# Kernel optimization log

Measured on AMD Instinct MI355X. Metric: run time of the kernel, lower is better.

The kernel has to match this reference:

```python
import jax, jax.numpy as jnp
import numpy as np

N_NODES = 100000
N_RELS = 1000
N_EDGES = 400000
DIM = 256  # even: split into real/imag halves


def setup_inputs() -> dict:
    key = jax.random.key(0)
    k1, k2, k3, k4, k5 = jax.random.split(key, 5)
    node_emb = jax.random.normal(k1, (N_NODES, DIM), dtype=jnp.float32)
    rel_emb = jax.random.normal(k2, (N_RELS, DIM), dtype=jnp.float32)
    src = jax.random.randint(k3, (N_EDGES,), 0, N_NODES, dtype=jnp.int64 if jax.config.jax_enable_x64 else jnp.int32).astype(jnp.int32)
    dst = jax.random.randint(k4, (N_EDGES,), 0, N_NODES).astype(jnp.int32)
    rel_id = jax.random.randint(k5, (N_EDGES,), 0, N_RELS).astype(jnp.int32)
    return {"node_emb": node_emb, "rel_emb": rel_emb, "src": src, "dst": dst, "rel_id": rel_id}


def reference(node_emb, rel_emb, src, dst, rel_id):
    h = node_emb[src]      # [E, D] gathered head embeddings
    t = node_emb[dst]      # [E, D] gathered tail embeddings
    r = rel_emb[rel_id]    # [E, D] gathered relation embeddings
    half = h.shape[-1] // 2
    rh, ih = h[:, :half], h[:, half:]
    rt, it = t[:, :half], t[:, half:]
    rr, ir = r[:, :half], r[:, half:]
    # ComplEx: Re(<h, r, conj(t)>)
    score = rh * rt * rr + ih * it * rr + rh * it * ir - ih * rt * ir
    return jnp.sum(score, axis=-1)  # [E]
```

## Files before the change

kernel.cpp:

```cpp
#include <hip/hip_runtime.h>
#include <hip/hip_fp16.h>
#include <string.h>

#define DIM 256

typedef __attribute__((ext_vector_type(2))) _Float16 half2v;

#if defined(__has_builtin)
#if __has_builtin(__builtin_amdgcn_fdot2)
#define HAVE_FDOT2 1
#endif
#endif

__global__ __launch_bounds__(256) void compress_f16i_kernel(
    const float* __restrict__ node, const float* __restrict__ rel,
    int4* __restrict__ out, int n_node, int n_total)
{
    int i = blockIdx.x * blockDim.x + threadIdx.x;
    int row = i >> 5;
    int q   = i & 31;
    if (row >= n_total) return;

    const float* base = (row < n_node)
        ? (node + (size_t)row * DIM)
        : (rel + (size_t)(row - n_node) * DIM);

    float4 a = *((const float4*)base + q);
    float4 b = *((const float4*)(base + 128) + q);

    __half2 p0 = __float22half2_rn(make_float2(a.x, b.x));
    __half2 p1 = __float22half2_rn(make_float2(a.y, b.y));
    __half2 p2 = __float22half2_rn(make_float2(a.z, b.z));
    __half2 p3 = __float22half2_rn(make_float2(a.w, b.w));

    int4 o;
    memcpy(&o.x, &p0, 4);
    memcpy(&o.y, &p1, 4);
    memcpy(&o.z, &p2, 4);
    memcpy(&o.w, &p3, 4);
    out[(size_t)row * 32 + q] = o;
}

__device__ __forceinline__ float pair_term(int h32, int t32, int r32, float acc)
{
    unsigned tu = (unsigned)t32;
    unsigned tsw = (tu >> 16) | ((tu << 16) ^ 0x80000000u);

    half2v h2, t2, r2, ts2;
    memcpy(&h2, &h32, 4);
    memcpy(&t2, &t32, 4);
    memcpy(&r2, &r32, 4);
    memcpy(&ts2, &tsw, 4);

#ifdef HAVE_FDOT2
    float u = __builtin_amdgcn_fdot2(r2, t2, 0.0f, false);
    float v = __builtin_amdgcn_fdot2(r2, ts2, 0.0f, false);
#else
    float rr = (float)r2.x, ir = (float)r2.y;
    float rt = (float)t2.x, it = (float)t2.y;
    float u = rr * rt + ir * it;
    float v = rr * it - ir * rt;
    (void)ts2;
#endif
    float rh = (float)h2.x;
    float ih = (float)h2.y;
    acc = fmaf(rh, u, acc);
    acc = fmaf(ih, v, acc);
    return acc;
}

__global__ __launch_bounds__(256) void complex_score_f16i4_kernel(
    const __half* __restrict__ node,
    const __half* __restrict__ rel,
    const int* __restrict__ src,
    const int* __restrict__ dst,
    const int* __restrict__ rid,
    float* __restrict__ out,
    int n_edges, int quarter)
{
    const int tid  = blockIdx.x * blockDim.x + threadIdx.x;
    const int g    = tid >> 5;
    const int lane = tid & 31;
    if (g >= quarter) return;

    int e[4];
    bool have[4];
    #pragma unroll
    for (int k = 0; k < 4; ++k) {
        e[k] = g + k * quarter;
        have[k] = (e[k] < n_edges);
    }

    int s[4], d[4], r[4];
    #pragma unroll
    for (int k = 0; k < 4; ++k) {
        int ek = have[k] ? e[k] : 0;
        s[k] = src[ek];
        d[k] = dst[ek];
        r[k] = rid[ek];
    }

    const int4* np = (const int4*)node;
    const int4* rp = (const int4*)rel;

    int4 hv[4], tv[4], vv[4];
    #pragma unroll
    for (int k = 0; k < 4; ++k) {
        hv[k] = np[(size_t)s[k] * 32 + lane];
        tv[k] = np[(size_t)d[k] * 32 + lane];
        vv[k] = rp[(size_t)r[k] * 32 + lane];
    }

    float acc[4];
    #pragma unroll
    for (int k = 0; k < 4; ++k) {
        float a = 0.0f;
        a = pair_term(hv[k].x, tv[k].x, vv[k].x, a);
        a = pair_term(hv[k].y, tv[k].y, vv[k].y, a);
        a = pair_term(hv[k].z, tv[k].z, vv[k].z, a);
        a = pair_term(hv[k].w, tv[k].w, vv[k].w, a);
        acc[k] = a;
    }

    #pragma unroll
    for (int off = 16; off > 0; off >>= 1) {
        #pragma unroll
        for (int k = 0; k < 4; ++k)
            acc[k] += __shfl_xor(acc[k], off);
    }

    if (lane == 0) {
        #pragma unroll
        for (int k = 0; k < 4; ++k)
            if (have[k]) out[e[k]] = acc[k];
    }
}

__global__ __launch_bounds__(256) void complex_score_f32_kernel(
    const float* __restrict__ node_emb,
    const float* __restrict__ rel_emb,
    const int* __restrict__ src,
    const int* __restrict__ dst,
    const int* __restrict__ rel_id,
    float* __restrict__ out,
    int n_edges)
{
    const int tid  = blockIdx.x * blockDim.x + threadIdx.x;
    const int edge = tid >> 5;
    const int lane = tid & 31;
    if (edge >= n_edges) return;

    const int s = src[edge];
    const int d = dst[edge];
    const int r = rel_id[edge];

    const float4* hp = (const float4*)(node_emb + (size_t)s * DIM);
    const float4* tp = (const float4*)(node_emb + (size_t)d * DIM);
    const float4* rp = (const float4*)(rel_emb  + (size_t)r * DIM);

    float4 rh = hp[lane];
    float4 ih = hp[lane + 32];
    float4 rt = tp[lane];
    float4 it = tp[lane + 32];
    float4 rr = rp[lane];
    float4 ir = rp[lane + 32];

    float a0 = rr.x * (rh.x * rt.x + ih.x * it.x) + ir.x * (rh.x * it.x - ih.x * rt.x);
    float a1 = rr.y * (rh.y * rt.y + ih.y * it.y) + ir.y * (rh.y * it.y - ih.y * rt.y);
    float a2 = rr.z * (rh.z * rt.z + ih.z * it.z) + ir.z * (rh.z * it.z - ih.z * rt.z);
    float a3 = rr.w * (rh.w * rt.w + ih.w * it.w) + ir.w * (rh.w * it.w - ih.w * rt.w);
    float acc = (a0 + a1) + (a2 + a3);

    #pragma unroll
    for (int off = 16; off > 0; off >>= 1)
        acc += __shfl_xor(acc, off, 32);

    if (lane == 0)
        out[edge] = acc;
}

extern "C" void kernel_launch(void* const* d_in, const int* in_sizes, int n_in,
                              void* d_out, int out_size, void* d_ws, size_t ws_size,
                              hipStream_t stream) {
    const float* node_emb = (const float*)d_in[0];
    const float* rel_emb  = (const float*)d_in[1];
    const int*   src      = (const int*)d_in[2];
    const int*   dst      = (const int*)d_in[3];
    const int*   rel_id   = (const int*)d_in[4];
    float* out = (float*)d_out;

    const int n_edges = in_sizes[2];
    const int n_nodes = in_sizes[0] / DIM;
    const int n_rels  = in_sizes[1] / DIM;

    const size_t f16_bytes = ((size_t)n_nodes + (size_t)n_rels) * DIM * 2;
    const int tpb = 256;

    if (ws_size >= f16_bytes) {
        __half* node_f16 = (__half*)d_ws;
        __half* rel_f16  = node_f16 + (size_t)n_nodes * DIM;

        const int n_total_rows = n_nodes + n_rels;
        const long long comp_threads = (long long)n_total_rows * 32;
        compress_f16i_kernel<<<(int)((comp_threads + tpb - 1) / tpb), tpb, 0, stream>>>(
            node_emb, rel_emb, (int4*)d_ws, n_nodes, n_total_rows);

        const int quarter = (n_edges + 3) / 4;
        const long long score_threads = (long long)quarter * 32;
        complex_score_f16i4_kernel<<<(int)((score_threads + tpb - 1) / tpb), tpb, 0, stream>>>(
            node_f16, rel_f16, src, dst, rel_id, out, n_edges, quarter);
    } else {
        const long long total_threads = (long long)n_edges * 32;
        complex_score_f32_kernel<<<(int)((total_threads + tpb - 1) / tpb), tpb, 0, stream>>>(
            node_emb, rel_emb, src, dst, rel_id, out, n_edges);
    }
}
```

Before: 219.0 us.

## Bucket edges by source node range before scoring to improve gather locality

Adds a coarse counting sort of edges by the high bits of the source index (histogram, scan, scatter into packed int4 records holding src, dst, rel and original edge id). The scoring kernel then reads the packed records, so edges processed close together touch nearby head rows, aiming for better L2/MALL hit rates on the gathers. In exchange it launches four extra small kernels and an extra pass over the index arrays. Only the head gather gains locality; tail and relation gathers stay random.

```diff
diff --git a/kernel.cpp b/kernel.cpp
--- a/kernel.cpp
+++ b/kernel.cpp
@@ -3,6 +3,7 @@
 #include <string.h>
 
 #define DIM 256
+#define CHUNK 2048
 
 typedef __attribute__((ext_vector_type(2))) _Float16 half2v;
 
@@ -39,6 +40,85 @@
     memcpy(&o.z, &p2, 4);
     memcpy(&o.w, &p3, 4);
     out[(size_t)row * 32 + q] = o;
+}
+
+__global__ void zero_cnt_kernel(unsigned* __restrict__ cnt, int nb)
+{
+    int i = threadIdx.x;
+    if (i < nb) cnt[i] = 0u;
+}
+
+__global__ __launch_bounds__(256) void hist_kernel(
+    const int* __restrict__ src, unsigned* __restrict__ cnt,
+    int n_edges, int shift, int nb)
+{
+    __shared__ unsigned lh[64];
+    int tid = threadIdx.x;
+    if (tid < 64) lh[tid] = 0u;
+    __syncthreads();
+
+    int base = blockIdx.x * CHUNK;
+    #pragma unroll
+    for (int i = 0; i < CHUNK / 256; ++i) {
+        int e = base + i * 256 + tid;
+        if (e < n_edges) {
+            int b = src[e] >> shift;
+            atomicAdd(&lh[b], 1u);
+        }
+    }
+    __syncthreads();
+    if (tid < nb && lh[tid]) atomicAdd(&cnt[tid], lh[tid]);
+}
+
+__global__ void scan_kernel(const unsigned* __restrict__ cnt,
+                            unsigned* __restrict__ cursors, int nb)
+{
+    int lane = threadIdx.x;
+    unsigned v = (lane < nb) ? cnt[lane] : 0u;
+    unsigned x = v;
+    #pragma unroll
+    for (int off = 1; off < 64; off <<= 1) {
+        unsigned y = __shfl_up(x, off);
+        if (lane >= off) x += y;
+    }
+    if (lane < nb) cursors[lane] = x - v;
+}
+
+__global__ __launch_bounds__(256) void scatter_kernel(
+    const int* __restrict__ src, const int* __restrict__ dst,
+    const int* __restrict__ rid, unsigned* __restrict__ cursors,
+    int4* __restrict__ packed, int n_edges, int shift, int nb)
+{
+    __shared__ unsigned lh[64];
+    __shared__ unsigned lbase[64];
+    int tid = threadIdx.x;
+    if (tid < 64) lh[tid] = 0u;
+    __syncthreads();
+
+    int base = blockIdx.x * CHUNK;
+    #pragma unroll
+    for (int i = 0; i < CHUNK / 256; ++i) {
+        int e = base + i * 256 + tid;
+        if (e < n_edges) atomicAdd(&lh[src[e] >> shift], 1u);
+    }
+    __syncthreads();
+    if (tid < 64) {
+        unsigned c = lh[tid];
+        lbase[tid] = (tid < nb && c) ? atomicAdd(&cursors[tid], c) : 0u;
+        lh[tid] = 0u;
+    }
+    __syncthreads();
+    #pragma unroll
+    for (int i = 0; i < CHUNK / 256; ++i) {
+        int e = base + i * 256 + tid;
+        if (e < n_edges) {
+            int s = src[e];
+            int b = s >> shift;
+            unsigned rank = atomicAdd(&lh[b], 1u);
+            unsigned pos = lbase[b] + rank;
+            packed[pos] = make_int4(s, dst[e], rid[e], e);
+        }
+    }
 }
 
 __device__ __forceinline__ float pair_term(int h32, int t32, int r32, float acc)
@@ -69,6 +149,68 @@
     return acc;
 }
 
+__global__ __launch_bounds__(256) void complex_score_f16p_kernel(
+    const __half* __restrict__ node,
+    const __half* __restrict__ rel,
+    const int4* __restrict__ packed,
+    float* __restrict__ out,
+    int n_edges, int groups)
+{
+    const int tid  = blockIdx.x * blockDim.x + threadIdx.x;
+    const int g    = tid >> 5;
+    const int lane = tid & 31;
+    if (g >= groups) return;
+
+    int eidx = 4 * g + (lane & 3);
+    int4 pk = packed[min(eidx, n_edges - 1)];
+
+    int s[4], d[4], r[4], eo[4];
+    bool have[4];
+    #pragma unroll
+    for (int k = 0; k < 4; ++k) {
+        s[k]  = __shfl(pk.x, k, 4);
+        d[k]  = __shfl(pk.y, k, 4);
+        r[k]  = __shfl(pk.z, k, 4);
+        eo[k] = __shfl(pk.w, k, 4);
+        have[k] = (4 * g + k < n_edges);
+    }
+
+    const int4* np = (const int4*)node;
+    const int4* rp = (const int4*)rel;
+
+    int4 hv[4], tv[4], vv[4];
+    #pragma unroll
+    for (int k = 0; k < 4; ++k) {
+        hv[k] = np[(size_t)s[k] * 32 + lane];
+        tv[k] = np[(size_t)d[k] * 32 + lane];
+        vv[k] = rp[(size_t)r[k] * 32 + lane];
+    }
+
+    float acc[4];
+    #pragma unroll
+    for (int k = 0; k < 4; ++k) {
+        float a = 0.0f;
+        a = pair_term(hv[k].x, tv[k].x, vv[k].x, a);
+        a = pair_term(hv[k].y, tv[k].y, vv[k].y, a);
+        a = pair_term(hv[k].z, tv[k].z, vv[k].z, a);
+        a = pair_term(hv[k].w, tv[k].w, vv[k].w, a);
+        acc[k] = a;
+    }
+
+    #pragma unroll
+    for (int off = 16; off > 0; off >>= 1) {
+        #pragma unroll
+        for (int k = 0; k < 4; ++k)
+            acc[k] += __shfl_xor(acc[k], off);
+    }
+
+    if (lane == 0) {
+        #pragma unroll
+        for (int k = 0; k < 4; ++k)
+            if (have[k]) out[eo[k]] = acc[k];
+    }
+}
+
 __global__ __launch_bounds__(256) void complex_score_f16i4_kernel(
     const __half* __restrict__ node,
     const __half* __restrict__ rel,
@@ -83,26 +225,17 @@
     const int lane = tid & 31;
     if (g >= quarter) return;
 
-    int e[4];
-    bool have[4];
-    #pragma unroll
-    for (int k = 0; k < 4; ++k) {
-        e[k] = g + k * quarter;
-        have[k] = (e[k] < n_edges);
-    }
-
+    int e[4]; bool have[4];
+    #pragma unroll
+    for (int k = 0; k < 4; ++k) { e[k] = g + k * quarter; have[k] = (e[k] < n_edges); }
     int s[4], d[4], r[4];
     #pragma unroll
     for (int k = 0; k < 4; ++k) {
         int ek = have[k] ? e[k] : 0;
-        s[k] = src[ek];
-        d[k] = dst[ek];
-        r[k] = rid[ek];
-    }
-
+        s[k] = src[ek]; d[k] = dst[ek]; r[k] = rid[ek];
+    }
     const int4* np = (const int4*)node;
     const int4* rp = (const int4*)rel;
-
     int4 hv[4], tv[4], vv[4];
     #pragma unroll
     for (int k = 0; k < 4; ++k) {
@@ -110,7 +243,6 @@
         tv[k] = np[(size_t)d[k] * 32 + lane];
         vv[k] = rp[(size_t)r[k] * 32 + lane];
     }
-
     float acc[4];
     #pragma unroll
     for (int k = 0; k < 4; ++k) {
@@ -121,18 +253,14 @@
         a = pair_term(hv[k].w, tv[k].w, vv[k].w, a);
         acc[k] = a;
     }
-
     #pragma unroll
     for (int off = 16; off > 0; off >>= 1) {
         #pragma unroll
-        for (int k = 0; k < 4; ++k)
-            acc[k] += __shfl_xor(acc[k], off);
-    }
-
+        for (int k = 0; k < 4; ++k) acc[k] += __shfl_xor(acc[k], off);
+    }
     if (lane == 0) {
         #pragma unroll
-        for (int k = 0; k < 4; ++k)
-            if (have[k]) out[e[k]] = acc[k];
+        for (int k = 0; k < 4; ++k) if (have[k]) out[e[k]] = acc[k];
     }
 }
 
@@ -193,10 +321,40 @@
     const int n_nodes = in_sizes[0] / DIM;
     const int n_rels  = in_sizes[1] / DIM;
 
-    const size_t f16_bytes = ((size_t)n_nodes + (size_t)n_rels) * DIM * 2;
+    const size_t F = ((size_t)n_nodes + (size_t)n_rels) * DIM * 2;
+    const size_t P = (size_t)n_edges * 16;
+    const size_t need_full = F + P + 2 * 64 * sizeof(unsigned);
     const int tpb = 256;
 
-    if (ws_size >= f16_bytes) {
+    int shift = 12;
+    while ((((n_nodes - 1) >> shift) + 1) > 64) ++shift;
+    const int nb = ((n_nodes - 1) >> shift) + 1;
+
+    if (ws_size >= need_full) {
+        __half*   node_f16 = (__half*)d_ws;
+        __half*   rel_f16  = node_f16 + (size_t)n_nodes * DIM;
+        int4*     packed   = (int4*)((char*)d_ws + F);
+        unsigned* cnt      = (unsigned*)((char*)d_ws + F + P);
+        unsigned* cursors  = cnt + 64;
+
+        const int n_total_rows = n_nodes + n_rels;
+        const long long comp_threads = (long long)n_total_rows * 32;
+        compress_f16i_kernel<<<(int)((comp_threads + tpb - 1) / tpb), tpb, 0, stream>>>(
+            node_emb, rel_emb, (int4*)d_ws, n_nodes, n_total_rows);
+
+        zero_cnt_kernel<<<1, 64, 0, stream>>>(cnt, nb);
+
+        const int chunks = (n_edges + CHUNK - 1) / CHUNK;
+        hist_kernel<<<chunks, tpb, 0, stream>>>(src, cnt, n_edges, shift, nb);
+        scan_kernel<<<1, 64, 0, stream>>>(cnt, cursors, nb);
+        scatter_kernel<<<chunks, tpb, 0, stream>>>(
+            src, dst, rel_id, cursors, packed, n_edges, shift, nb);
+
+        const int groups = (n_edges + 3) / 4;
+        const long long score_threads = (long long)groups * 32;
+        complex_score_f16p_kernel<<<(int)((score_threads + tpb - 1) / tpb), tpb, 0, stream>>>(
+            node_f16, rel_f16, packed, out, n_edges, groups);
+    } else if (ws_size >= F) {
         __half* node_f16 = (__half*)d_ws;
         __half* rel_f16  = node_f16 + (size_t)n_nodes * DIM;
 
```

After: 237.7 us. 8.5% more time.
